# Kernel optimization log

Measured on AMD Instinct MI355X. Metric: run time of the kernel, lower is better.

The kernel has to match this reference:

```python
import jax, jax.numpy as jnp
import numpy as np

N_HEAD = 12
M_HIST = 5      # Anderson history window (AndersonAcceleration.m)
BETA = 1.0      # Anderson mixing (AndersonAcceleration.beta)
LN_EPS = 1e-5


def _layer_norm(x, w, b):
    mu = x.mean(-1, keepdims=True)
    xc = x - mu
    var = (xc * xc).mean(-1, keepdims=True)
    return xc * jax.lax.rsqrt(var + LN_EPS) * w + b


def _mha(x, wqkv, bqkv, wo, bo):
    # torch nn.MultiheadAttention, batch_first, self-attention, no mask, dropout=0
    B, T, C = x.shape
    dh = C // N_HEAD
    qkv = x @ wqkv.T + bqkv                       # [B,T,3C]
    q, k, v = jnp.split(qkv, 3, axis=-1)
    def heads(t):
        return t.reshape(B, T, N_HEAD, dh).transpose(0, 2, 1, 3)  # [B,H,T,dh]
    q, k, v = heads(q), heads(k), heads(v)
    scores = jnp.einsum('bhqd,bhkd->bhqk', q, k) / jnp.sqrt(jnp.asarray(dh, x.dtype))
    att = jax.nn.softmax(scores, axis=-1)
    out = jnp.einsum('bhqk,bhkd->bhqd', att, v).transpose(0, 2, 1, 3).reshape(B, T, C)
    return out @ wo.T + bo


def _deq_delta(z, u, emb_row, ln1_w, ln1_b, in_proj_w, in_proj_b, out_proj_w,
               out_proj_b, ln2_w, ln2_b, mlp_w1, mlp_b1, mlp_w2, mlp_b2):
    # DEQOperator.forward -> delta_z
    z_temporal = z + 0.1 * emb_row                 # broadcast [C] over [B,T,C]
    z_ctx = z_temporal + u
    x = _layer_norm(z_ctx, ln1_w, ln1_b)
    attn_out = _mha(x, in_proj_w, in_proj_b, out_proj_w, out_proj_b)
    z_attn = z + attn_out
    h = _layer_norm(z_attn, ln2_w, ln2_b)
    h = jax.nn.gelu(h @ mlp_w1.T + mlp_b1, approximate=False) @ mlp_w2.T + mlp_b2
    z_mlp = z_attn + h
    return z_mlp - z


def _deq_solve(u, iter_emb, ln1_w, ln1_b, in_proj_w, in_proj_b, out_proj_w,
               out_proj_b, ln2_w, ln2_b, mlp_w1, mlp_b1, mlp_w2, mlp_b2, num_iters):
    B, T, C = u.shape
    z = jnp.zeros_like(u)
    Xs, Fs = [], []   # Anderson history of states / residuals
    max_row = iter_emb.shape[0] - 1
    for it in range(num_iters):
        emb_row = iter_emb[min(it, max_row)]
        delta = _deq_delta(z, u, emb_row, ln1_w, ln1_b, in_proj_w, in_proj_b,
                           out_proj_w, out_proj_b, ln2_w, ln2_b,
                           mlp_w1, mlp_b1, mlp_w2, mlp_b2)
        res = delta  # residual of f(z) = z + delta_z w.r.t. z
        Xs.append(z); Fs.append(res)
        if len(Xs) > M_HIST:
            Xs.pop(0); Fs.pop(0)
        if len(Xs) == 1:
            z = z + BETA * res
        else:
            K = len(Xs) - 1
            dF = jnp.stack(Fs[:-1], 0) - res[None]               # [K,B,T,C]
            dF_f = dF.transpose(1, 2, 0, 3).reshape(B * T, K, C)  # per-token LS
            r_f = res.reshape(B * T, C)
            G = jnp.einsum('nkc,nlc->nkl', dF_f, dF_f)            # [BT,K,K]
            G = G + 1e-6 * jnp.eye(K, dtype=u.dtype)
            bvec = jnp.einsum('nkc,nc->nk', dF_f, r_f)            # [BT,K]
            alpha = jnp.linalg.solve(G, bvec[..., None])[..., 0]
            d = r_f - jnp.einsum('nkc,nk->nc', dF_f, alpha)
            z = (z.reshape(B * T, C) + BETA * d).reshape(B, T, C)
    return z


def setup_inputs() -> dict:
    key = jax.random.key(0)
    ks = jax.random.split(key, 6)
    B, T, C = 4, 1024, 768
    std = 0.02
    return {
        'u': jax.random.normal(ks[0], (B, T, C), jnp.float32),
        'iter_emb': std * jax.random.normal(ks[1], (31, C), jnp.float32),
        'ln1_w': jnp.ones((C,), jnp.float32),
        'ln1_b': jnp.zeros((C,), jnp.float32),
        'in_proj_w': std * jax.random.normal(ks[2], (3 * C, C), jnp.float32),
        'in_proj_b': jnp.zeros((3 * C,), jnp.float32),
        'out_proj_w': std * jax.random.normal(ks[3], (C, C), jnp.float32),
        'out_proj_b': jnp.zeros((C,), jnp.float32),
        'ln2_w': jnp.ones((C,), jnp.float32),
        'ln2_b': jnp.zeros((C,), jnp.float32),
        'mlp_w1': std * jax.random.normal(ks[4], (4 * C, C), jnp.float32),
        'mlp_b1': jnp.zeros((4 * C,), jnp.float32),
        'mlp_w2': std * jax.random.normal(ks[5], (C, 4 * C), jnp.float32),
        'mlp_b2': jnp.zeros((C,), jnp.float32),
        'num_iters': 6,
    }


def reference(u, iter_emb, ln1_w, ln1_b, in_proj_w, in_proj_b, out_proj_w,
              out_proj_b, ln2_w, ln2_b, mlp_w1, mlp_b1, mlp_w2, mlp_b2, num_iters):
    return _deq_solve(u, iter_emb, ln1_w, ln1_b, in_proj_w, in_proj_b,
                      out_proj_w, out_proj_b, ln2_w, ln2_b,
                      mlp_w1, mlp_b1, mlp_w2, mlp_b2, int(num_iters))
```

## Files before the change

kernel.cpp:

```cpp
#include <hip/hip_runtime.h>
#include <math.h>

#define BT 4096
#define CDIM 768
#define NHEAD 12
#define DH 64
#define TSEQ 1024
#define BBATCH 4

typedef _Float16 f16;
typedef __attribute__((ext_vector_type(4))) _Float16 f16x4;
typedef __attribute__((ext_vector_type(8))) _Float16 f16x8;
typedef __attribute__((ext_vector_type(4))) float f32x4;

__device__ __forceinline__ void gload_lds16(const f16* g, f16* l) {
  __builtin_amdgcn_global_load_lds(
      (const __attribute__((address_space(1))) unsigned*)(const void*)g,
      (__attribute__((address_space(3))) unsigned*)(void*)l, 16, 0, 0);
}

__device__ __forceinline__ float block_reduce_sum(float v, float* sbuf) {
#pragma unroll
  for (int o = 32; o > 0; o >>= 1) v += __shfl_down(v, o, 64);
  int lane = threadIdx.x & 63;
  int w = threadIdx.x >> 6;
  if (lane == 0) sbuf[w] = v;
  __syncthreads();
  float r = sbuf[0] + sbuf[1] + sbuf[2] + sbuf[3];
  __syncthreads();
  return r;
}

__global__ __launch_bounds__(256) void zero_kernel(float4* __restrict__ p) {
  p[(size_t)blockIdx.x * 256 + threadIdx.x] = make_float4(0.f, 0.f, 0.f, 0.f);
}

__global__ __launch_bounds__(256) void cvt_f16_kernel(
    const float* __restrict__ in, f16* __restrict__ out) {
  size_t i = ((size_t)blockIdx.x * 256 + threadIdx.x) * 4;
  float4 v = *(const float4*)(in + i);
  f16x4 o = {(f16)v.x, (f16)v.y, (f16)v.z, (f16)v.w};
  *(f16x4*)(out + i) = o;
}

__global__ __launch_bounds__(256) void ln1_kernel(
    const float* __restrict__ z, const float* __restrict__ u,
    const float* __restrict__ emb, const float* __restrict__ w,
    const float* __restrict__ b, f16* __restrict__ x) {
  __shared__ float sbuf[4];
  int row = blockIdx.x;
  int tid = threadIdx.x;
  const float* zr = z + (size_t)row * CDIM;
  const float* ur = u + (size_t)row * CDIM;
  float v[3];
  float s = 0.f;
#pragma unroll
  for (int i = 0; i < 3; i++) {
    int c = tid + i * 256;
    v[i] = zr[c] + 0.1f * emb[c] + ur[c];
    s += v[i];
  }
  s = block_reduce_sum(s, sbuf);
  float mu = s * (1.f / CDIM);
  float sq = 0.f;
#pragma unroll
  for (int i = 0; i < 3; i++) { v[i] -= mu; sq += v[i] * v[i]; }
  sq = block_reduce_sum(sq, sbuf);
  float rstd = rsqrtf(sq * (1.f / CDIM) + 1e-5f);
  f16* xr = x + (size_t)row * CDIM;
#pragma unroll
  for (int i = 0; i < 3; i++) {
    int c = tid + i * 256;
    xr[c] = (f16)(v[i] * rstd * w[c] + b[c]);
  }
}

__global__ __launch_bounds__(256) void ln2_kernel(
    const float* __restrict__ in, const float* __restrict__ w,
    const float* __restrict__ b, f16* __restrict__ x) {
  __shared__ float sbuf[4];
  int row = blockIdx.x;
  int tid = threadIdx.x;
  const float* ir = in + (size_t)row * CDIM;
  float v[3];
  float s = 0.f;
#pragma unroll
  for (int i = 0; i < 3; i++) {
    int c = tid + i * 256;
    v[i] = ir[c];
    s += v[i];
  }
  s = block_reduce_sum(s, sbuf);
  float mu = s * (1.f / CDIM);
  float sq = 0.f;
#pragma unroll
  for (int i = 0; i < 3; i++) { v[i] -= mu; sq += v[i] * v[i]; }
  sq = block_reduce_sum(sq, sbuf);
  float rstd = rsqrtf(sq * (1.f / CDIM) + 1e-5f);
  f16* xr = x + (size_t)row * CDIM;
#pragma unroll
  for (int i = 0; i < 3; i++) {
    int c = tid + i * 256;
    xr[c] = (f16)(v[i] * rstd * w[c] + b[c]);
  }
}

__device__ __forceinline__ float gelu_exact(float t) {
  return 0.5f * t * (1.f + erff(t * 0.70710678118654752f));
}

template <int MODE>
__global__ __launch_bounds__(256, 3) void gemm_mfma(
    const f16* __restrict__ A, const f16* __restrict__ W,
    const float* __restrict__ bias, f16* __restrict__ hq,
    f16* __restrict__ hk, f16* __restrict__ hvt, f16* __restrict__ hout,
    int M, int N, int K) {
  __shared__ __align__(16) f16 As[128 * 32];
  __shared__ __align__(16) f16 Bs[128 * 32];
  int tid = threadIdx.x;
  int wv = tid >> 6, lane = tid & 63;
  int bm = blockIdx.y, bn = blockIdx.x;
  int wm = (wv >> 1) * 64, wn = (wv & 1) * 64;

  int srow = wv * 16 + (lane >> 2);
  int scol = (lane & 3) * 8;
  const f16* gA = A + (size_t)(bm * 128 + srow) * K + scol;
  const f16* gB = W + (size_t)(bn * 128 + srow) * K + scol;
  f16* lA = As + wv * 16 * 32;
  f16* lB = Bs + wv * 16 * 32;

  f32x4 acc[4][4];
#pragma unroll
  for (int i = 0; i < 4; i++)
#pragma unroll
    for (int j = 0; j < 4; j++) acc[i][j] = (f32x4){0.f, 0.f, 0.f, 0.f};

  int arow = lane & 15;
  int koff = (lane >> 4) * 8;

  for (int k0 = 0; k0 < K; k0 += 32) {
    __syncthreads();
    gload_lds16(gA + k0, lA);
    gload_lds16(gA + (size_t)64 * K + k0, lA + 64 * 32);
    gload_lds16(gB + k0, lB);
    gload_lds16(gB + (size_t)64 * K + k0, lB + 64 * 32);
    __syncthreads();
    f16x8 af[4], bfr[4];
#pragma unroll
    for (int mi = 0; mi < 4; mi++)
      af[mi] = *(const f16x8*)&As[(wm + mi * 16 + arow) * 32 + koff];
#pragma unroll
    for (int nj = 0; nj < 4; nj++)
      bfr[nj] = *(const f16x8*)&Bs[(wn + nj * 16 + arow) * 32 + koff];
#pragma unroll
    for (int mi = 0; mi < 4; mi++)
#pragma unroll
      for (int nj = 0; nj < 4; nj++)
        acc[mi][nj] = __builtin_amdgcn_mfma_f32_16x16x32_f16(
            af[mi], bfr[nj], acc[mi][nj], 0, 0, 0);
  }

  int crow0 = bm * 128 + wm + (lane >> 4) * 4;
  int ccol0 = bn * 128 + wn + (lane & 15);
#pragma unroll
  for (int nj = 0; nj < 4; nj++) {
    int col = ccol0 + nj * 16;
    float bcol = bias[col];
    if constexpr (MODE == 3) {
      int which = col / CDIM;
      int rem = col - which * CDIM;
      int h = rem >> 6;
      int d = rem & 63;
#pragma unroll
      for (int mi = 0; mi < 4; mi++) {
#pragma unroll
        for (int r = 0; r < 4; r++) {
          int m = crow0 + mi * 16 + r;
          int bb = m >> 10, t = m & 1023;
          f16 val = (f16)(acc[mi][nj][r] + bcol);
          if (which == 0)
            hq[(((size_t)(bb * NHEAD + h) * TSEQ + t) << 6) + d] = val;
          else if (which == 1)
            hk[(((size_t)(bb * NHEAD + h) * TSEQ + t) << 6) + d] = val;
          else
            hvt[(((size_t)(bb * NHEAD + h) * DH + d) << 10) + t] = val;
        }
      }
    } else {
#pragma unroll
      for (int mi = 0; mi < 4; mi++) {
#pragma unroll
        for (int r = 0; r < 4; r++) {
          int m = crow0 + mi * 16 + r;
          size_t idx = (size_t)m * N + col;
          hout[idx] = (f16)gelu_exact(acc[mi][nj][r] + bcol);
        }
      }
    }
  }
}

template <int MODE>
__global__ __launch_bounds__(256, 4) void gemm_mfma64(
    const f16* __restrict__ A, const f16* __restrict__ W,
    const float* __restrict__ bias, const float* __restrict__ aux1,
    const float* __restrict__ aux2, float* __restrict__ fout0,
    int M, int N, int K) {
  __shared__ __align__(16) f16 As[64 * 32];
  __shared__ __align__(16) f16 Bs[64 * 32];
  int tid = threadIdx.x;
  int wv = tid >> 6, lane = tid & 63;
  int bm = blockIdx.y, bn = blockIdx.x;
  int wm = (wv >> 1) * 32, wn = (wv & 1) * 32;

  int srow = wv * 16 + (lane >> 2);
  int scol = (lane & 3) * 8;
  const f16* gA = A + (size_t)(bm * 64 + srow) * K + scol;
  const f16* gB = W + (size_t)(bn * 64 + srow) * K + scol;
  f16* lA = As + wv * 16 * 32;
  f16* lB = Bs + wv * 16 * 32;

  f32x4 acc[2][2];
#pragma unroll
  for (int i = 0; i < 2; i++)
#pragma unroll
    for (int j = 0; j < 2; j++) acc[i][j] = (f32x4){0.f, 0.f, 0.f, 0.f};

  int arow = lane & 15;
  int koff = (lane >> 4) * 8;

  for (int k0 = 0; k0 < K; k0 += 32) {
    __syncthreads();
    gload_lds16(gA + k0, lA);
    gload_lds16(gB + k0, lB);
    __syncthreads();
    f16x8 af[2], bfr[2];
#pragma unroll
    for (int mi = 0; mi < 2; mi++)
      af[mi] = *(const f16x8*)&As[(wm + mi * 16 + arow) * 32 + koff];
#pragma unroll
    for (int nj = 0; nj < 2; nj++)
      bfr[nj] = *(const f16x8*)&Bs[(wn + nj * 16 + arow) * 32 + koff];
#pragma unroll
    for (int mi = 0; mi < 2; mi++)
#pragma unroll
      for (int nj = 0; nj < 2; nj++)
        acc[mi][nj] = __builtin_amdgcn_mfma_f32_16x16x32_f16(
            af[mi], bfr[nj], acc[mi][nj], 0, 0, 0);
  }

  int crow0 = bm * 64 + wm + (lane >> 4) * 4;
  int ccol0 = bn * 64 + wn + (lane & 15);
#pragma unroll
  for (int nj = 0; nj < 2; nj++) {
    int col = ccol0 + nj * 16;
    float bcol = bias[col];
#pragma unroll
    for (int mi = 0; mi < 2; mi++) {
#pragma unroll
      for (int r = 0; r < 4; r++) {
        int m = crow0 + mi * 16 + r;
        size_t idx = (size_t)m * N + col;
        float val = acc[mi][nj][r] + bcol;
        if constexpr (MODE == 0) {
          fout0[idx] = val + aux1[idx];
        } else {
          fout0[idx] = val + aux1[idx] - aux2[idx];
        }
      }
    }
  }
}

#define PSTRIDE 72
#define KVS 72
__global__ __launch_bounds__(256, 3) void flash_attn8(
    const f16* __restrict__ Qg, const f16* __restrict__ Kg,
    const f16* __restrict__ Vt, f16* __restrict__ attn) {
  __shared__ __align__(16) f16 Ks[64 * KVS];
  __shared__ __align__(16) f16 Vs[64 * KVS];
  __shared__ __align__(16) f16 Plds[4][16 * PSTRIDE];
  int tid = threadIdx.x;
  int wv = tid >> 6, lane = tid & 63;
  int bh = blockIdx.x;
  int bb = bh / NHEAD, h = bh % NHEAD;
  int m0 = (blockIdx.y * 4 + wv) * 16;
  int am = lane & 15;
  int quad = lane >> 4;
  int ak = quad * 8;

  int srow = tid >> 3;
  int scol = (tid & 7) * 8;

  const f16* kb = Kg + (((size_t)bh * TSEQ) << 6);
  const f16* vb = Vt + (((size_t)bh * DH) << 10);

  const f16* qbase = Qg + (((size_t)bh * TSEQ + m0) << 6);
  f16x8 qf0 = *(const f16x8*)(qbase + am * 64 + ak);
  f16x8 qf1 = *(const f16x8*)(qbase + am * 64 + 32 + ak);
#pragma unroll
  for (int i = 0; i < 8; i++) { qf0[i] *= (f16)0.125f; qf1[i] *= (f16)0.125f; }

  f16* Pw = Plds[wv];
  f32x4 Oa[4];
#pragma unroll
  for (int i = 0; i < 4; i++) Oa[i] = (f32x4){0.f, 0.f, 0.f, 0.f};
  float lpart[4] = {0.f, 0.f, 0.f, 0.f};

  f16x8 kr0 = *(const f16x8*)(kb + (size_t)srow * 64 + scol);
  f16x8 kr1 = *(const f16x8*)(kb + (size_t)(32 + srow) * 64 + scol);
  f16x8 vr0 = *(const f16x8*)(vb + (size_t)srow * TSEQ + scol);
  f16x8 vr1 = *(const f16x8*)(vb + (size_t)(32 + srow) * TSEQ + scol);

  for (int n0 = 0; n0 < TSEQ; n0 += 64) {
    __syncthreads();
    *(f16x8*)&Ks[srow * KVS + scol] = kr0;
    *(f16x8*)&Ks[(32 + srow) * KVS + scol] = kr1;
    *(f16x8*)&Vs[srow * KVS + scol] = vr0;
    *(f16x8*)&Vs[(32 + srow) * KVS + scol] = vr1;
    __syncthreads();
    int nn = n0 + 64;
    if (nn < TSEQ) {
      kr0 = *(const f16x8*)(kb + (size_t)(nn + srow) * 64 + scol);
      kr1 = *(const f16x8*)(kb + (size_t)(nn + 32 + srow) * 64 + scol);
      vr0 = *(const f16x8*)(vb + (size_t)srow * TSEQ + nn + scol);
      vr1 = *(const f16x8*)(vb + (size_t)(32 + srow) * TSEQ + nn + scol);
    }
    f32x4 S[4];
#pragma unroll
    for (int t = 0; t < 4; t++) {
      f16x8 kf0 = *(const f16x8*)&Ks[(16 * t + am) * KVS + ak];
      f16x8 kf1 = *(const f16x8*)&Ks[(16 * t + am) * KVS + 32 + ak];
      S[t] = __builtin_amdgcn_mfma_f32_16x16x32_f16(
          qf0, kf0, (f32x4){0.f, 0.f, 0.f, 0.f}, 0, 0, 0);
      S[t] = __builtin_amdgcn_mfma_f32_16x16x32_f16(qf1, kf1, S[t], 0, 0, 0);
    }
#pragma unroll
    for (int t = 0; t < 4; t++) {
#pragma unroll
      for (int r = 0; r < 4; r++) {
        float p = __expf(S[t][r]);
        lpart[r] += p;
        Pw[(quad * 4 + r) * PSTRIDE + 16 * t + am] = (f16)p;
      }
    }
    f16x8 pa0 = *(const f16x8*)&Pw[am * PSTRIDE + ak];
    f16x8 pa1 = *(const f16x8*)&Pw[am * PSTRIDE + 32 + ak];
#pragma unroll
    for (int dt = 0; dt < 4; dt++) {
      f16x8 vf0 = *(const f16x8*)&Vs[(16 * dt + am) * KVS + ak];
      f16x8 vf1 = *(const f16x8*)&Vs[(16 * dt + am) * KVS + 32 + ak];
      Oa[dt] = __builtin_amdgcn_mfma_f32_16x16x32_f16(pa0, vf0, Oa[dt], 0, 0, 0);
      Oa[dt] = __builtin_amdgcn_mfma_f32_16x16x32_f16(pa1, vf1, Oa[dt], 0, 0, 0);
    }
  }

#pragma unroll
  for (int o = 1; o < 16; o <<= 1)
#pragma unroll
    for (int r = 0; r < 4; r++) lpart[r] += __shfl_xor(lpart[r], o, 64);

#pragma unroll
  for (int r = 0; r < 4; r++) {
    int m = m0 + quad * 4 + r;
    float inv = 1.f / lpart[r];
    f16* orow = attn + ((size_t)(bb * TSEQ + m)) * CDIM + h * DH;
#pragma unroll
    for (int dt = 0; dt < 4; dt++)
      orow[dt * 16 + am] = (f16)(Oa[dt][r] * inv);
  }
}

__global__ __launch_bounds__(256) void add_res_kernel(
    float* __restrict__ z, const float* __restrict__ r) {
  size_t i = (size_t)blockIdx.x * 256 + threadIdx.x;
  z[i] += r[i];
}

template <int KA>
__global__ __launch_bounds__(256) void anderson_kernel(
    float* __restrict__ z, const float* __restrict__ rescur,
    const float* __restrict__ p0, const float* __restrict__ p1,
    const float* __restrict__ p2, const float* __restrict__ p3) {
  __shared__ float sbuf[4];
  int row = blockIdx.x, tid = threadIdx.x;
  size_t base = (size_t)row * CDIM + tid;
  float r[3];
#pragma unroll
  for (int i = 0; i < 3; i++) r[i] = rescur[base + i * 256];
  const float* ps[4] = {p0, p1, p2, p3};
  float dF[KA][3];
#pragma unroll
  for (int k = 0; k < KA; k++)
#pragma unroll
    for (int i = 0; i < 3; i++) dF[k][i] = ps[k][base + i * 256] - r[i];

  float Gm[KA][KA], bv[KA];
#pragma unroll
  for (int k = 0; k < KA; k++) {
#pragma unroll
    for (int ll = k; ll < KA; ll++) {
      float p = 0.f;
#pragma unroll
      for (int i = 0; i < 3; i++) p += dF[k][i] * dF[ll][i];
      float t = block_reduce_sum(p, sbuf);
      Gm[k][ll] = t;
      Gm[ll][k] = t;
    }
  }
#pragma unroll
  for (int k = 0; k < KA; k++) Gm[k][k] += 1e-6f;
#pragma unroll
  for (int k = 0; k < KA; k++) {
    float p = 0.f;
#pragma unroll
    for (int i = 0; i < 3; i++) p += dF[k][i] * r[i];
    bv[k] = block_reduce_sum(p, sbuf);
  }
  float alpha[KA];
#pragma unroll
  for (int p = 0; p < KA; p++) {
    float inv = 1.f / Gm[p][p];
#pragma unroll
    for (int rr = p + 1; rr < KA; rr++) {
      float f = Gm[rr][p] * inv;
#pragma unroll
      for (int c = p; c < KA; c++) Gm[rr][c] -= f * Gm[p][c];
      bv[rr] -= f * bv[p];
    }
  }
#pragma unroll
  for (int p = KA - 1; p >= 0; p--) {
    float s2 = bv[p];
#pragma unroll
    for (int c = p + 1; c < KA; c++) s2 -= Gm[p][c] * alpha[c];
    alpha[p] = s2 / Gm[p][p];
  }
#pragma unroll
  for (int i = 0; i < 3; i++) {
    float d = r[i];
#pragma unroll
    for (int k = 0; k < KA; k++) d = fmaf(-dF[k][i], alpha[k], d);
    z[base + i * 256] += d;
  }
}

extern "C" void kernel_launch(void* const* d_in, const int* in_sizes, int n_in,
                              void* d_out, int out_size, void* d_ws,
                              size_t ws_size, hipStream_t stream) {
  (void)in_sizes; (void)n_in; (void)out_size; (void)ws_size;
  const float* u = (const float*)d_in[0];
  const float* iter_emb = (const float*)d_in[1];
  const float* ln1w = (const float*)d_in[2];
  const float* ln1b = (const float*)d_in[3];
  const float* wqkv = (const float*)d_in[4];
  const float* bqkv = (const float*)d_in[5];
  const float* wo = (const float*)d_in[6];
  const float* bo = (const float*)d_in[7];
  const float* ln2w = (const float*)d_in[8];
  const float* ln2b = (const float*)d_in[9];
  const float* w1 = (const float*)d_in[10];
  const float* b1 = (const float*)d_in[11];
  const float* w2 = (const float*)d_in[12];
  const float* b2 = (const float*)d_in[13];

  const size_t S = (size_t)BT * CDIM;
  float* ws = (float*)d_ws;
  float* z = ws + 0 * S;
  float* zattn = ws + 1 * S;
  float* res[5] = {ws + 2 * S, ws + 3 * S, ws + 4 * S, ws + 5 * S, ws + 6 * S};
  f16* q_h = (f16*)(ws + 7 * S);
  f16* k_h = q_h + S;
  f16* vt_h = q_h + 2 * S;
  f16* h_h = (f16*)(ws + 7 * S);
  f16* x_h = (f16*)(ws + 9 * S);
  f16* wqkv_h = x_h + S;
  f16* wo_h = wqkv_h + (size_t)3 * CDIM * CDIM;
  f16* w1_h = wo_h + (size_t)CDIM * CDIM;
  f16* w2_h = w1_h + (size_t)4 * CDIM * CDIM;

  cvt_f16_kernel<<<1728, 256, 0, stream>>>(wqkv, wqkv_h);
  cvt_f16_kernel<<<576, 256, 0, stream>>>(wo, wo_h);
  cvt_f16_kernel<<<2304, 256, 0, stream>>>(w1, w1_h);
  cvt_f16_kernel<<<2304, 256, 0, stream>>>(w2, w2_h);
  zero_kernel<<<S / 1024, 256, 0, stream>>>((float4*)z);

  for (int it = 0; it < 6; it++) {
    ln1_kernel<<<BT, 256, 0, stream>>>(z, u, iter_emb + it * CDIM, ln1w, ln1b,
                                       x_h);
    gemm_mfma<3><<<dim3(18, 32), 256, 0, stream>>>(
        x_h, wqkv_h, bqkv, q_h, k_h, vt_h, nullptr, BT, 3 * CDIM, CDIM);
    flash_attn8<<<dim3(BBATCH * NHEAD, TSEQ / 64), 256, 0, stream>>>(
        q_h, k_h, vt_h, x_h);
    gemm_mfma64<0><<<dim3(12, 64), 256, 0, stream>>>(
        x_h, wo_h, bo, z, nullptr, zattn, BT, CDIM, CDIM);
    ln2_kernel<<<BT, 256, 0, stream>>>(zattn, ln2w, ln2b, x_h);
    gemm_mfma<1><<<dim3(24, 32), 256, 0, stream>>>(
        x_h, w1_h, b1, nullptr, nullptr, nullptr, h_h, BT, 4 * CDIM, CDIM);
    float* rcur = res[it % 5];
    gemm_mfma64<2><<<dim3(12, 64), 256, 0, stream>>>(
        h_h, w2_h, b2, zattn, z, rcur, BT, CDIM, 4 * CDIM);

    int Kh = it < 4 ? it : 4;
    if (Kh == 0) {
      add_res_kernel<<<S / 256, 256, 0, stream>>>(z, rcur);
    } else {
      const float* p[4] = {rcur, rcur, rcur, rcur};
      for (int kx = 1; kx <= Kh; kx++) p[kx - 1] = res[(it - kx) % 5];
      switch (Kh) {
        case 1: anderson_kernel<1><<<BT, 256, 0, stream>>>(z, rcur, p[0], p[1], p[2], p[3]); break;
        case 2: anderson_kernel<2><<<BT, 256, 0, stream>>>(z, rcur, p[0], p[1], p[2], p[3]); break;
        case 3: anderson_kernel<3><<<BT, 256, 0, stream>>>(z, rcur, p[0], p[1], p[2], p[3]); break;
        default: anderson_kernel<4><<<BT, 256, 0, stream>>>(z, rcur, p[0], p[1], p[2], p[3]); break;
      }
    }
  }
  hipMemcpyAsync(d_out, z, S * sizeof(float), hipMemcpyDeviceToDevice, stream);
}
```

Measured before the change: 1.374 ms.

## Register-prefetch and pad LDS tiles in 64x64 GEMM, deepen K-step, swap grid order

The 64x64 MFMA GEMM used for the output projection and MLP down-projection now loads the next K tile into registers while computing the current one. It uses a K step of 64 instead of 32 and writes into padded LDS rows (stride 72) to reduce bank conflicts, replacing direct global-to-LDS loads. The grid is transposed so that consecutive blocks walk along M for the same weight column tile, which may improve L2 reuse of the weights. This costs extra registers and LDS per block, which may reduce occupancy.

```diff
diff --git a/kernel.cpp b/kernel.cpp
--- a/kernel.cpp
+++ b/kernel.cpp
@@ -200,25 +200,24 @@
   }
 }
 
+#define GS 72
 template <int MODE>
 __global__ __launch_bounds__(256, 4) void gemm_mfma64(
     const f16* __restrict__ A, const f16* __restrict__ W,
     const float* __restrict__ bias, const float* __restrict__ aux1,
     const float* __restrict__ aux2, float* __restrict__ fout0,
     int M, int N, int K) {
-  __shared__ __align__(16) f16 As[64 * 32];
-  __shared__ __align__(16) f16 Bs[64 * 32];
+  __shared__ __align__(16) f16 As[64 * GS];
+  __shared__ __align__(16) f16 Bs[64 * GS];
   int tid = threadIdx.x;
   int wv = tid >> 6, lane = tid & 63;
-  int bm = blockIdx.y, bn = blockIdx.x;
+  int bm = blockIdx.x, bn = blockIdx.y;
   int wm = (wv >> 1) * 32, wn = (wv & 1) * 32;
 
-  int srow = wv * 16 + (lane >> 2);
-  int scol = (lane & 3) * 8;
+  int srow = tid >> 2;
+  int scol = (tid & 3) * 16;
   const f16* gA = A + (size_t)(bm * 64 + srow) * K + scol;
   const f16* gB = W + (size_t)(bn * 64 + srow) * K + scol;
-  f16* lA = As + wv * 16 * 32;
-  f16* lB = Bs + wv * 16 * 32;
 
   f32x4 acc[2][2];
 #pragma unroll
@@ -226,27 +225,44 @@
 #pragma unroll
     for (int j = 0; j < 2; j++) acc[i][j] = (f32x4){0.f, 0.f, 0.f, 0.f};
 
-  int arow = lane & 15;
-  int koff = (lane >> 4) * 8;
-
-  for (int k0 = 0; k0 < K; k0 += 32) {
+  int am = lane & 15;
+  int ak = (lane >> 4) * 8;
+
+  f16x8 a0 = *(const f16x8*)(gA);
+  f16x8 a1 = *(const f16x8*)(gA + 8);
+  f16x8 b0 = *(const f16x8*)(gB);
+  f16x8 b1 = *(const f16x8*)(gB + 8);
+
+  for (int k0 = 0; k0 < K; k0 += 64) {
     __syncthreads();
-    gload_lds16(gA + k0, lA);
-    gload_lds16(gB + k0, lB);
+    *(f16x8*)&As[srow * GS + scol] = a0;
+    *(f16x8*)&As[srow * GS + scol + 8] = a1;
+    *(f16x8*)&Bs[srow * GS + scol] = b0;
+    *(f16x8*)&Bs[srow * GS + scol + 8] = b1;
     __syncthreads();
-    f16x8 af[2], bfr[2];
-#pragma unroll
-    for (int mi = 0; mi < 2; mi++)
-      af[mi] = *(const f16x8*)&As[(wm + mi * 16 + arow) * 32 + koff];
-#pragma unroll
-    for (int nj = 0; nj < 2; nj++)
-      bfr[nj] = *(const f16x8*)&Bs[(wn + nj * 16 + arow) * 32 + koff];
-#pragma unroll
-    for (int mi = 0; mi < 2; mi++)
+    int kn = k0 + 64;
+    if (kn < K) {
+      a0 = *(const f16x8*)(gA + kn);
+      a1 = *(const f16x8*)(gA + kn + 8);
+      b0 = *(const f16x8*)(gB + kn);
+      b1 = *(const f16x8*)(gB + kn + 8);
+    }
+#pragma unroll
+    for (int kk = 0; kk < 2; kk++) {
+      f16x8 af[2], bfr[2];
+#pragma unroll
+      for (int mi = 0; mi < 2; mi++)
+        af[mi] = *(const f16x8*)&As[(wm + mi * 16 + am) * GS + kk * 32 + ak];
 #pragma unroll
       for (int nj = 0; nj < 2; nj++)
-        acc[mi][nj] = __builtin_amdgcn_mfma_f32_16x16x32_f16(
-            af[mi], bfr[nj], acc[mi][nj], 0, 0, 0);
+        bfr[nj] = *(const f16x8*)&Bs[(wn + nj * 16 + am) * GS + kk * 32 + ak];
+#pragma unroll
+      for (int mi = 0; mi < 2; mi++)
+#pragma unroll
+        for (int nj = 0; nj < 2; nj++)
+          acc[mi][nj] = __builtin_amdgcn_mfma_f32_16x16x32_f16(
+              af[mi], bfr[nj], acc[mi][nj], 0, 0, 0);
+    }
   }
 
   int crow0 = bm * 64 + wm + (lane >> 4) * 4;
@@ -492,13 +508,13 @@
         x_h, wqkv_h, bqkv, q_h, k_h, vt_h, nullptr, BT, 3 * CDIM, CDIM);
     flash_attn8<<<dim3(BBATCH * NHEAD, TSEQ / 64), 256, 0, stream>>>(
         q_h, k_h, vt_h, x_h);
-    gemm_mfma64<0><<<dim3(12, 64), 256, 0, stream>>>(
+    gemm_mfma64<0><<<dim3(64, 12), 256, 0, stream>>>(
         x_h, wo_h, bo, z, nullptr, zattn, BT, CDIM, CDIM);
     ln2_kernel<<<BT, 256, 0, stream>>>(zattn, ln2w, ln2b, x_h);
     gemm_mfma<1><<<dim3(24, 32), 256, 0, stream>>>(
         x_h, w1_h, b1, nullptr, nullptr, nullptr, h_h, BT, 4 * CDIM, CDIM);
     float* rcur = res[it % 5];
-    gemm_mfma64<2><<<dim3(12, 64), 256, 0, stream>>>(
+    gemm_mfma64<2><<<dim3(64, 12), 256, 0, stream>>>(
         h_h, w2_h, b2, zattn, z, rcur, BT, CDIM, 4 * CDIM);
 
     int Kh = it < 4 ? it : 4;
```

After: 1.243 ms. 9.5% less time.
